# Performance work log

Hardware: AMD Instinct MI355X
Metric: run time of the kernel (lower is better)

The kernel has to match this reference:

```python
import jax, jax.numpy as jnp
import numpy as np


def setup_inputs() -> dict:
    key = jax.random.key(0)
    ks = jax.random.split(key, 8)
    T, S, W, O = 50000, 168, 336, 48
    N = T - W - O + 1
    x = jax.random.uniform(ks[0], (T,), minval=0.5, maxval=1.5, dtype=jnp.float32)
    noise = jax.random.normal(ks[1], (N, W), dtype=jnp.float32) * 0.001  # Normal(0, std=0.001)
    level_sc = jax.random.uniform(ks[2], (), minval=-1.0, maxval=1.0, dtype=jnp.float32)
    seas_sc = jax.random.uniform(ks[3], (), minval=-1.0, maxval=1.0, dtype=jnp.float32)
    init_seas = jax.random.uniform(ks[4], (S,), minval=0.65, maxval=1.35, dtype=jnp.float32)
    W1 = jax.random.normal(ks[5], (W, W), dtype=jnp.float32) / np.float32(np.sqrt(W))
    b1 = jnp.zeros((W,), jnp.float32)
    W2 = jax.random.normal(ks[6], (W, O), dtype=jnp.float32) / np.float32(np.sqrt(W))
    b2 = jnp.zeros((O,), jnp.float32)
    return {"x": x, "noise": noise, "level_sc": level_sc, "seas_sc": seas_sc,
            "init_seas": init_seas, "W1": W1, "b1": b1, "W2": W2, "b2": b2,
            "window_size": W, "out_size": O, "lvp": 1}


def reference(x, noise, level_sc, seas_sc, init_seas, W1, b1, W2, b2,
              window_size, out_size, lvp):
    T = x.shape[0]
    a = jax.nn.sigmoid(level_sc)      # level smoothing coeff
    g = jax.nn.sigmoid(seas_sc)       # seasonal smoothing coeff
    s0 = jnp.exp(init_seas)           # [S] initial multiplicative seasonals
    # seasonals list in torch: seas[0..S-1]=s0, seas[S]=s0[0], seas[S+i]=w_i.
    # Ring buffer holds seas[i..i+S-1] at step i (starting i=1): [s0[1:], s0[0]].
    buf0 = jnp.concatenate([s0[1:], s0[:1]])
    level0 = x[0] / s0[0]

    def step(carry, xi):
        level, buf = carry
        seas_i = buf[0]
        new_level = a * xi / seas_i + (1.0 - a) * level
        new_w = g * xi / new_level + (1.0 - g) * seas_i
        new_buf = jnp.concatenate([buf[1:], new_w[None]])
        return (new_level, new_buf), (new_level, new_w, jnp.log(new_level / level))

    _, (lvls, ws, logdiffs) = jax.lax.scan(step, (level0, buf0), x[1:])
    levels = jnp.concatenate([level0[None], lvls])        # [T]
    seas_full = jnp.concatenate([s0, s0[:1], ws])         # [S+T]

    d = logdiffs[1:] - logdiffs[:-1]
    level_var_loss = jnp.mean(d * d) * lvp

    N = T - window_size - out_size + 1
    idx_in = jnp.arange(N)[:, None] + jnp.arange(window_size)[None, :]   # [N,W]
    idx_lab = jnp.arange(N)[:, None] + window_size + jnp.arange(out_size)[None, :]  # [N,O]
    lev = levels[jnp.arange(N) + window_size][:, None]    # [N,1]
    inp = jnp.log(x[idx_in] / (lev * seas_full[idx_in])) + noise   # noisy squashed inputs
    labels = jnp.log(x[idx_lab] / (lev * seas_full[idx_lab]))

    h = jnp.tanh(inp @ W1 + b1)        # tanh_no_lstm: Linear(336,336)+tanh
    out = h @ W2 + b2                  # linear_no_lstm: Linear(336,48)
    return out, labels, level_var_loss
```

## Files before the change

### kernel.cpp

```cpp
#include <hip/hip_runtime.h>
#include <hip/hip_bf16.h>

typedef __attribute__((ext_vector_type(8))) short  s16x8;
typedef __attribute__((ext_vector_type(4))) short  s16x4;
typedef __attribute__((ext_vector_type(4))) float  f32x4;

#define T_LEN 50000
#define S_LEN 168
#define W_IN  336
#define O_OUT 48
#define N_ROWS (T_LEN - W_IN - O_OUT + 1)
#define N_PAD  49664
#define NBLK   (N_PAD / 64)

__device__ inline short f2bf(float f) {
    union { float f; unsigned u; } v; v.f = f;
    unsigned u = v.u;
    unsigned r = u + 0x7fffu + ((u >> 16) & 1u);
    return (short)(r >> 16);
}

__device__ inline int bfpk(float lo, float hi) {
    float2 f2; f2.x = lo; f2.y = hi;
    __hip_bfloat162 h = __float22bfloat162_rn(f2);
    int r; __builtin_memcpy(&r, &h, 4);
    return r;
}

__device__ inline float readlane_f(float v, int l) {
    return __int_as_float(__builtin_amdgcn_readlane(__float_as_int(v), l));
}

__device__ inline float fast_tanh(float v) {
    float e = __expf(2.f * v);
    return 1.f - 2.f * __builtin_amdgcn_rcpf(e + 1.f);
}

__global__ void k_preconvert(const float* __restrict__ W1, const float* __restrict__ W2,
                             short* __restrict__ W1T, short* __restrict__ W2T,
                             float* __restrict__ S1) {
    int idx = blockIdx.x * 256 + threadIdx.x;
    const int n1 = 352 * 352;
    const int n2 = n1 + 48 * 360;
    if (idx < n1) {
        int j = idx / 352, k = idx % 352;
        W1T[idx] = (j < 336 && k < 336) ? f2bf(W1[k * 336 + j]) : (short)0;
    } else if (idx < n2) {
        int i2 = idx - n1;
        int o = i2 / 360, k = i2 % 360;
        W2T[i2] = (k < 336) ? f2bf(W2[k * 48 + o]) : (short)0;
    } else if (idx < n2 + 352) {
        int j = idx - n2;
        float s = 0.f;
        if (j < 336)
            for (int k = 0; k < 336; ++k) s += W1[k * 336 + j];
        S1[j] = s;
    }
}

#define DPP_FMA(q_, CTRL, W, RM) { \
    int t_ = __builtin_amdgcn_update_dpp(0, __float_as_int(q_), (CTRL), (RM), 0xf, true); \
    q_ = fmaf((W), __int_as_float(t_), q_); }

__global__ void k_scan(const float* __restrict__ x, const float* __restrict__ level_sc,
                       const float* __restrict__ seas_sc, const float* __restrict__ init_seas,
                       float* __restrict__ lw, float* __restrict__ seasinit) {
    int lane = threadIdx.x;
    float a = 1.f / (1.f + expf(-level_sc[0]));
    float g = 1.f / (1.f + expf(-seas_sc[0]));
    float om = 1.f - a, omg = 1.f - g;

    for (int t = lane; t <= S_LEN; t += 64)
        seasinit[t] = expf(init_seas[t < S_LEN ? t : 0]);

    float lpv = x[0] / expf(init_seas[0]);
    if (lane == 0) { lw[0] = lpv; lw[1] = 1.f; }

    float om1 = om, om2v = om1 * om1, om4 = om2v * om2v, om8 = om4 * om4;
    float pl    = powf(om, (float)(lane + 1));
    float fpre  = powf(om, (float)((lane & 15) + 1));
    float fpre2 = powf(om, (float)((lane & 31) + 1));

    int  idx4 = ((lane + 24) & 63) << 2;
    bool lowj = (lane < 40);

#define SCAN(QOUT, XV, RSV) { \
    float q_ = a * (XV) * (RSV); \
    DPP_FMA(q_, 0x111, om1,  0xf); \
    DPP_FMA(q_, 0x112, om2v, 0xf); \
    DPP_FMA(q_, 0x114, om4,  0xf); \
    DPP_FMA(q_, 0x118, om8,  0xf); \
    DPP_FMA(q_, 0x142, fpre,  0xa); \
    DPP_FMA(q_, 0x143, fpre2, 0xc); \
    QOUT = q_; }

#define XLOAD(I) float xr##I = x[1 + 64 * I + lane];
    XLOAD(0) XLOAD(1) XLOAD(2) XLOAD(3) XLOAD(4) XLOAD(5) XLOAD(6) XLOAD(7)
    XLOAD(8) XLOAD(9) XLOAD(10) XLOAD(11) XLOAD(12) XLOAD(13) XLOAD(14) XLOAD(15)
#undef XLOAD

    float sW = expf(init_seas[1 + lane]);
    float sN = expf(init_seas[65 + lane]);
    int t105 = 105 + lane;
    float wPrev = expf(init_seas[t105 >= S_LEN ? 0 : t105]);
    float Qcur; SCAN(Qcur, xr0, __builtin_amdgcn_rcpf(sW));
    int ib = 1;

#define BODY(R, RN, CLAMP) { \
    float lvl = fmaf(pl, lpv, Qcur); \
    lpv = readlane_f(lvl, 63); \
    float w_ = fmaf(omg, sW, (g * xr##R) * __builtin_amdgcn_rcpf(lvl)); \
    float2 pk_; pk_.x = lvl; pk_.y = w_; \
    *(float2*)&lw[2 * (ib + lane)] = pk_; \
    int tA_ = __builtin_amdgcn_ds_bpermute(idx4, __float_as_int(wPrev)); \
    int tB_ = __builtin_amdgcn_ds_bpermute(idx4, __float_as_int(w_)); \
    float sNN_ = lowj ? __int_as_float(tA_) : __int_as_float(tB_); \
    float Qn_; SCAN(Qn_, xr##RN, __builtin_amdgcn_rcpf(sN)); \
    int pidx = ib + 1024 + lane; \
    if (CLAMP) pidx = pidx > (T_LEN - 1) ? (T_LEN - 1) : pidx; \
    xr##R = x[pidx]; \
    Qcur = Qn_; sW = sN; sN = sNN_; wPrev = w_; \
    ib += 64; }

    for (int kb = 0; kb < 47; ++kb) {
        BODY(0,1,0)  BODY(1,2,0)  BODY(2,3,0)  BODY(3,4,0)
        BODY(4,5,0)  BODY(5,6,0)  BODY(6,7,0)  BODY(7,8,0)
        BODY(8,9,0)  BODY(9,10,0) BODY(10,11,0) BODY(11,12,0)
        BODY(12,13,0) BODY(13,14,0) BODY(14,15,0) BODY(15,0,0)
    }
    BODY(0,1,0)  BODY(1,2,0)  BODY(2,3,0)  BODY(3,4,0)
    BODY(4,5,0)  BODY(5,6,0)  BODY(6,7,0)  BODY(7,8,0)
    BODY(8,9,0)  BODY(9,10,0) BODY(10,11,0) BODY(11,12,0)
    BODY(12,13,0)
    BODY(13,14,1) BODY(14,15,1) BODY(15,0,1)
    BODY(0,1,1)  BODY(1,2,1)  BODY(2,3,1)  BODY(3,4,1)
    BODY(4,5,1)  BODY(5,6,1)  BODY(6,7,1)  BODY(7,8,1)
    BODY(8,9,1)  BODY(9,10,1) BODY(10,11,1) BODY(11,12,1)
#undef BODY

    {
        float lvl = fmaf(pl, lpv, Qcur);
        lpv = readlane_f(lvl, 63);
        float w_ = fmaf(omg, sW, (g * xr12) * __builtin_amdgcn_rcpf(lvl));
        float2 pk_; pk_.x = lvl; pk_.y = w_;
        *(float2*)&lw[2 * (49921 + lane)] = pk_;
    }
    {
        float Qn_; SCAN(Qn_, xr13, __builtin_amdgcn_rcpf(sN));
        float lvl = fmaf(pl, lpv, Qn_);
        if (lane < 15) {
            float w_ = fmaf(omg, sN, (g * xr13) * __builtin_amdgcn_rcpf(lvl));
            float2 pk_; pk_.x = lvl; pk_.y = w_;
            *(float2*)&lw[2 * (49985 + lane)] = pk_;
        }
    }
#undef SCAN
}

__global__ void k_logs(const float* __restrict__ x, const float* __restrict__ lw,
                       const float* __restrict__ seasinit,
                       float* __restrict__ F, float* __restrict__ llev,
                       float* __restrict__ partials) {
    __shared__ float sm[258];
    __shared__ float red[256];
    int tid = threadIdx.x;
    int t = blockIdx.x * 256 + tid;
    float ll = 0.f;
    if (t < T_LEN) {
        float2 cur = *(const float2*)&lw[2 * t];
        int ps = t - S_LEN; if (ps < 0) ps = 0;
        float sv = (t <= S_LEN) ? seasinit[t] : lw[2 * ps + 1];
        F[t]  = __logf(x[t]) - __logf(sv);
        ll    = __logf(cur.x);
        llev[t] = ll;
    }
    sm[tid] = ll;
    if (tid < 2) {
        int te = blockIdx.x * 256 + 256 + tid;
        sm[256 + tid] = (te < T_LEN) ? __logf(lw[2 * te]) : 0.f;
    }
    __syncthreads();
    float s = 0.f;
    if (t < T_LEN - 2) {
        float d = sm[tid + 2] - 2.f * sm[tid + 1] + sm[tid];
        s = d * d;
    }
    red[tid] = s; __syncthreads();
    for (int off = 128; off > 0; off >>= 1) {
        if (tid < off) red[tid] += red[tid + off];
        __syncthreads();
    }
    if (tid == 0) partials[blockIdx.x] = red[0];
}

__global__ __launch_bounds__(512, 4) void k_gemm(
        const float* __restrict__ noise, const float* __restrict__ F,
        const float* __restrict__ llev, const short* __restrict__ W1T,
        const float* __restrict__ b1, const short* __restrict__ W2T,
        const float* __restrict__ b2, const float* __restrict__ S1,
        const float* __restrict__ partials, const int* __restrict__ lvp,
        float* __restrict__ out, float* __restrict__ labels, float* __restrict__ loss) {
    __shared__ __align__(16) short hlds[64][360];
    __shared__ __align__(16) float Flds[448];
    __shared__ __align__(16) float Llds[64];
    __shared__ __align__(16) float b1lds[352];
    __shared__ __align__(16) float S1lds[352];

    int t = threadIdx.x, w = t >> 6, l = t & 63;
    int lm = l & 15, lq = l >> 4;
    long n0 = (long)blockIdx.x * 64;

    if (blockIdx.x == 0 && w == 7) {
        float s = partials[l] + partials[l + 64] + partials[l + 128];
        if (l < 4) s += partials[l + 192];
#pragma unroll
        for (int off = 32; off > 0; off >>= 1) s += __shfl_down(s, off, 64);
        if (l == 0) loss[0] = s / (float)(T_LEN - 2) * (float)lvp[0];
    }

    if (t < 112)      *(f32x4*)&Flds[t * 4] = *(const f32x4*)&F[n0 + t * 4];
    else if (t < 128) *(f32x4*)&Llds[(t - 112) * 4] = *(const f32x4*)&llev[n0 + W_IN + (t - 112) * 4];
    else if (t < 216) {
        int i4 = (t - 128) * 4;
        f32x4 v = (f32x4){0.f, 0.f, 0.f, 0.f};
        if (i4 < W_IN) v = *(const f32x4*)&b1[i4];
        *(f32x4*)&b1lds[i4] = v;
    } else if (t < 304) {
        int i4 = (t - 216) * 4;
        *(f32x4*)&S1lds[i4] = *(const f32x4*)&S1[i4];
    }

    int rbase = (w >> 1) * 16;
    int jbase = (w & 1) * 176;
    long an0 = n0 + rbase + lm; if (an0 > N_ROWS - 2) an0 = N_ROWS - 2;
    const float* nr0 = noise + an0 * W_IN + lq * 8;

    f32x4 nc0 = *(const f32x4*)&nr0[0], nc1 = *(const f32x4*)&nr0[4];

    f32x4 acc[11];
#pragma unroll
    for (int c = 0; c < 11; ++c) acc[c] = (f32x4){0.f, 0.f, 0.f, 0.f};

    const short* w1row = &W1T[(jbase + lm) * 352 + lq * 8];
#define LDW(CT, KS) (*(const s16x8*)&w1row[(CT) * 5632 + (KS) * 32])
    s16x8 af0 = LDW(0,0), af1 = LDW(1,0), af2 = LDW(2,0), af3 = LDW(3,0), af4 = LDW(4,0),
          af5 = LDW(5,0), af6 = LDW(6,0), af7 = LDW(7,0), af8 = LDW(8,0), af9 = LDW(9,0),
          af10 = LDW(10,0);

    __syncthreads();

#define MM(CT, AF) acc[CT] = __builtin_amdgcn_mfma_f32_16x16x32_bf16(AF, bf0, acc[CT], 0, 0, 0);

#define KSTEP(KS) { \
    s16x8 bf0; \
    { int fb = rbase + lm + (KS) * 32 + lq * 8; \
      int* b0i = (int*)&bf0; \
      b0i[0] = bfpk(Flds[fb+0] + nc0[0], Flds[fb+1] + nc0[1]); \
      b0i[1] = bfpk(Flds[fb+2] + nc0[2], Flds[fb+3] + nc0[3]); \
      b0i[2] = bfpk(Flds[fb+4] + nc1[0], Flds[fb+5] + nc1[1]); \
      b0i[3] = bfpk(Flds[fb+6] + nc1[2], Flds[fb+7] + nc1[3]); } \
    if ((KS) < 10) { \
      nc0 = *(const f32x4*)&nr0[((KS)+1)*32]; \
      nc1 = *(const f32x4*)&nr0[((KS)+1)*32+4]; \
    } \
    MM(0, af0)   if ((KS) < 10) af0  = LDW(0,  (KS)+1); \
    MM(1, af1)   if ((KS) < 10) af1  = LDW(1,  (KS)+1); \
    MM(2, af2)   if ((KS) < 10) af2  = LDW(2,  (KS)+1); \
    MM(3, af3)   if ((KS) < 10) af3  = LDW(3,  (KS)+1); \
    MM(4, af4)   if ((KS) < 10) af4  = LDW(4,  (KS)+1); \
    MM(5, af5)   if ((KS) < 10) af5  = LDW(5,  (KS)+1); \
    MM(6, af6)   if ((KS) < 10) af6  = LDW(6,  (KS)+1); \
    MM(7, af7)   if ((KS) < 10) af7  = LDW(7,  (KS)+1); \
    MM(8, af8)   if ((KS) < 10) af8  = LDW(8,  (KS)+1); \
    MM(9, af9)   if ((KS) < 10) af9  = LDW(9,  (KS)+1); \
    MM(10, af10) if ((KS) < 10) af10 = LDW(10, (KS)+1); \
}

    KSTEP(0) KSTEP(1) KSTEP(2) KSTEP(3) KSTEP(4) KSTEP(5)
    KSTEP(6) KSTEP(7) KSTEP(8) KSTEP(9) KSTEP(10)
#undef KSTEP
#undef MM
#undef LDW

    float lv0 = Llds[rbase + lm];
#pragma unroll
    for (int ct = 0; ct < 11; ++ct) {
        f32x4 b1q = *(f32x4*)&b1lds[jbase + ct * 16 + lq * 4];
        f32x4 s1q = *(f32x4*)&S1lds[jbase + ct * 16 + lq * 4];
        int2 p0;
        p0.x = bfpk(fast_tanh(fmaf(-lv0, s1q[0], acc[ct][0] + b1q[0])),
                    fast_tanh(fmaf(-lv0, s1q[1], acc[ct][1] + b1q[1])));
        p0.y = bfpk(fast_tanh(fmaf(-lv0, s1q[2], acc[ct][2] + b1q[2])),
                    fast_tanh(fmaf(-lv0, s1q[3], acc[ct][3] + b1q[3])));
        *(int2*)&hlds[rbase + lm][jbase + ct * 16 + lq * 4] = p0;
    }
    __syncthreads();

    if (w < 4) {
        f32x4 a2[3];
        a2[0] = (f32x4){0,0,0,0}; a2[1] = (f32x4){0,0,0,0}; a2[2] = (f32x4){0,0,0,0};
#pragma unroll
        for (int ks = 0; ks < 11; ++ks) {
            s16x8 hf = *(s16x8*)&hlds[w * 16 + lm][ks * 32 + lq * 8];
#pragma unroll
            for (int ct = 0; ct < 3; ++ct) {
                s16x8 bf2 = *(const s16x8*)&W2T[(ct * 16 + lm) * 360 + ks * 32 + lq * 8];
                a2[ct] = __builtin_amdgcn_mfma_f32_16x16x32_bf16(hf, bf2, a2[ct], 0, 0, 0);
            }
        }
        int rloc = w * 16 + lq * 4;
#pragma unroll
        for (int ct = 0; ct < 3; ++ct) {
            float b2v = b2[ct * 16 + lm];
#pragma unroll
            for (int r = 0; r < 4; ++r) {
                long row = n0 + rloc + r;
                if (row < N_ROWS) out[row * O_OUT + ct * 16 + lm] = a2[ct][r] + b2v;
            }
        }
    } else {
        int rb2 = (w - 4) * 16;
        int lrow = l >> 2, cbase = (l & 3) * 12;
        long row = n0 + rb2 + lrow;
        if (row < N_ROWS) {
            float fl = -Llds[rb2 + lrow];
            const float* fp = &Flds[rb2 + lrow + W_IN + cbase];
            float* lp = &labels[row * O_OUT + cbase];
#pragma unroll
            for (int i = 0; i < 12; ++i) lp[i] = fp[i] + fl;
        }
    }
}

extern "C" void kernel_launch(void* const* d_in, const int* in_sizes, int n_in,
                              void* d_out, int out_size, void* d_ws, size_t ws_size,
                              hipStream_t stream) {
    const float* x         = (const float*)d_in[0];
    const float* noise     = (const float*)d_in[1];
    const float* level_sc  = (const float*)d_in[2];
    const float* seas_sc   = (const float*)d_in[3];
    const float* init_seas = (const float*)d_in[4];
    const float* W1        = (const float*)d_in[5];
    const float* b1        = (const float*)d_in[6];
    const float* W2        = (const float*)d_in[7];
    const float* b2        = (const float*)d_in[8];
    const int*   lvp       = (const int*)d_in[11];

    float* out    = (float*)d_out;
    float* labels = out + (long)N_ROWS * O_OUT;
    float* loss   = labels + (long)N_ROWS * O_OUT;

    float* wsf      = (float*)d_ws;
    float* lw       = wsf;
    float* seasinit = wsf + 100096;
    float* F        = wsf + 100288;
    float* llev     = wsf + 150464;
    float* partials = wsf + 200512;
    float* S1f      = wsf + 200768;
    short* W1T      = (short*)(wsf + 201152);
    short* W2T      = W1T + 352 * 352;

    k_preconvert<<<554, 256, 0, stream>>>(W1, W2, W1T, W2T, S1f);
    k_scan<<<1, 64, 0, stream>>>(x, level_sc, seas_sc, init_seas, lw, seasinit);
    k_logs<<<196, 256, 0, stream>>>(x, lw, seasinit, F, llev, partials);
    k_gemm<<<NBLK, 512, 0, stream>>>(noise, F, llev, W1T, b1, W2T, b2, S1f,
                                     partials, lvp, out, labels, loss);
}
```

Before: 162.0 us.

## Split input prep into separate bf16 materialization kernel and register-block GEMM over two row tiles

Adds a k_prep kernel that builds the noisy log inputs (level subtracted) as a padded bf16 matrix in workspace and writes labels. k_gemm then loads bf16 A fragments directly, uses 256 threads with each wave computing two 16-row tiles so every W1 fragment is reused across two MFMAs, and rotates six weight registers instead of eleven. The S1 column-sum correction is dropped because the level term is now folded into the input. This costs an extra global write and read of about 35 MB of bf16 input plus one more launch, in exchange for less conversion work inside the GEMM and less weight reload per row.

```diff
diff --git a/kernel.cpp b/kernel.cpp
--- a/kernel.cpp
+++ b/kernel.cpp
@@ -37,8 +37,7 @@
 }
 
 __global__ void k_preconvert(const float* __restrict__ W1, const float* __restrict__ W2,
-                             short* __restrict__ W1T, short* __restrict__ W2T,
-                             float* __restrict__ S1) {
+                             short* __restrict__ W1T, short* __restrict__ W2T) {
     int idx = blockIdx.x * 256 + threadIdx.x;
     const int n1 = 352 * 352;
     const int n2 = n1 + 48 * 360;
@@ -49,12 +48,6 @@
         int i2 = idx - n1;
         int o = i2 / 360, k = i2 % 360;
         W2T[i2] = (k < 336) ? f2bf(W2[k * 48 + o]) : (short)0;
-    } else if (idx < n2 + 352) {
-        int j = idx - n2;
-        float s = 0.f;
-        if (j < 336)
-            for (int k = 0; k < 336; ++k) s += W1[k * 336 + j];
-        S1[j] = s;
     }
 }
 
@@ -193,24 +186,66 @@
     if (tid == 0) partials[blockIdx.x] = red[0];
 }
 
-__global__ __launch_bounds__(512, 4) void k_gemm(
+__global__ __launch_bounds__(256) void k_prep(
         const float* __restrict__ noise, const float* __restrict__ F,
-        const float* __restrict__ llev, const short* __restrict__ W1T,
+        const float* __restrict__ llev, short* __restrict__ inpbf,
+        float* __restrict__ labels) {
+    __shared__ float Flds[448];
+    __shared__ float Llds[64];
+    int t = threadIdx.x;
+    long n0 = (long)blockIdx.x * 64;
+    if (t < 112)      *(f32x4*)&Flds[t * 4] = *(const f32x4*)&F[n0 + t * 4];
+    else if (t < 128) *(f32x4*)&Llds[(t - 112) * 4] = *(const f32x4*)&llev[n0 + W_IN + (t - 112) * 4];
+    __syncthreads();
+
+    int r = t >> 2, q = t & 3;
+    long n = n0 + r;
+    bool valid = (n < N_ROWS);
+    float lv = Llds[r];
+    const float* nrow = noise + n * (long)W_IN;
+    short* orow = inpbf + n * 352;
+
+#pragma unroll
+    for (int i = 0; i < 11; ++i) {
+        int k0 = q * 88 + i * 8;
+        int4 s = {0, 0, 0, 0};
+        if (valid && k0 < W_IN) {
+            f32x4 nz0 = *(const f32x4*)&nrow[k0];
+            f32x4 nz1 = *(const f32x4*)&nrow[k0 + 4];
+            const float* fp = &Flds[r + k0];
+            s.x = bfpk(fp[0] - lv + nz0[0], fp[1] - lv + nz0[1]);
+            s.y = bfpk(fp[2] - lv + nz0[2], fp[3] - lv + nz0[3]);
+            s.z = bfpk(fp[4] - lv + nz1[0], fp[5] - lv + nz1[1]);
+            s.w = bfpk(fp[6] - lv + nz1[2], fp[7] - lv + nz1[3]);
+        }
+        *(int4*)&orow[k0] = s;
+    }
+    if (valid) {
+#pragma unroll
+        for (int i = 0; i < 3; ++i) {
+            int c = q * 12 + i * 4;
+            const float* fp = &Flds[r + W_IN + c];
+            f32x4 v;
+            v[0] = fp[0] - lv; v[1] = fp[1] - lv; v[2] = fp[2] - lv; v[3] = fp[3] - lv;
+            *(f32x4*)&labels[n * O_OUT + c] = v;
+        }
+    }
+}
+
+__global__ __launch_bounds__(256, 3) void k_gemm(
+        const short* __restrict__ inpbf, const short* __restrict__ W1T,
         const float* __restrict__ b1, const short* __restrict__ W2T,
-        const float* __restrict__ b2, const float* __restrict__ S1,
-        const float* __restrict__ partials, const int* __restrict__ lvp,
-        float* __restrict__ out, float* __restrict__ labels, float* __restrict__ loss) {
+        const float* __restrict__ b2, const float* __restrict__ partials,
+        const int* __restrict__ lvp, float* __restrict__ out,
+        float* __restrict__ loss) {
     __shared__ __align__(16) short hlds[64][360];
-    __shared__ __align__(16) float Flds[448];
-    __shared__ __align__(16) float Llds[64];
     __shared__ __align__(16) float b1lds[352];
-    __shared__ __align__(16) float S1lds[352];
 
     int t = threadIdx.x, w = t >> 6, l = t & 63;
     int lm = l & 15, lq = l >> 4;
     long n0 = (long)blockIdx.x * 64;
 
-    if (blockIdx.x == 0 && w == 7) {
+    if (blockIdx.x == 0 && w == 3) {
         float s = partials[l] + partials[l + 64] + partials[l + 128];
         if (l < 4) s += partials[l + 192];
 #pragma unroll
@@ -218,116 +253,101 @@
         if (l == 0) loss[0] = s / (float)(T_LEN - 2) * (float)lvp[0];
     }
 
-    if (t < 112)      *(f32x4*)&Flds[t * 4] = *(const f32x4*)&F[n0 + t * 4];
-    else if (t < 128) *(f32x4*)&Llds[(t - 112) * 4] = *(const f32x4*)&llev[n0 + W_IN + (t - 112) * 4];
-    else if (t < 216) {
-        int i4 = (t - 128) * 4;
+    if (t < 88) {
+        int i4 = t * 4;
         f32x4 v = (f32x4){0.f, 0.f, 0.f, 0.f};
         if (i4 < W_IN) v = *(const f32x4*)&b1[i4];
         *(f32x4*)&b1lds[i4] = v;
-    } else if (t < 304) {
-        int i4 = (t - 216) * 4;
-        *(f32x4*)&S1lds[i4] = *(const f32x4*)&S1[i4];
-    }
-
-    int rbase = (w >> 1) * 16;
+    }
+
+    int rbase = (w >> 1) * 32;
     int jbase = (w & 1) * 176;
-    long an0 = n0 + rbase + lm; if (an0 > N_ROWS - 2) an0 = N_ROWS - 2;
-    const float* nr0 = noise + an0 * W_IN + lq * 8;
-
-    f32x4 nc0 = *(const f32x4*)&nr0[0], nc1 = *(const f32x4*)&nr0[4];
-
-    f32x4 acc[11];
-#pragma unroll
-    for (int c = 0; c < 11; ++c) acc[c] = (f32x4){0.f, 0.f, 0.f, 0.f};
+    const short* arow0 = inpbf + (n0 + rbase + lm) * 352 + lq * 8;
+    const short* arow1 = arow0 + 16 * 352;
+
+    f32x4 acc0[11], acc1[11];
+#pragma unroll
+    for (int c = 0; c < 11; ++c) { acc0[c] = (f32x4){0,0,0,0}; acc1[c] = (f32x4){0,0,0,0}; }
 
     const short* w1row = &W1T[(jbase + lm) * 352 + lq * 8];
 #define LDW(CT, KS) (*(const s16x8*)&w1row[(CT) * 5632 + (KS) * 32])
-    s16x8 af0 = LDW(0,0), af1 = LDW(1,0), af2 = LDW(2,0), af3 = LDW(3,0), af4 = LDW(4,0),
-          af5 = LDW(5,0), af6 = LDW(6,0), af7 = LDW(7,0), af8 = LDW(8,0), af9 = LDW(9,0),
-          af10 = LDW(10,0);
+    s16x8 af0 = LDW(0,0), af1 = LDW(1,0), af2 = LDW(2,0),
+          af3 = LDW(3,0), af4 = LDW(4,0), af5 = LDW(5,0);
+    s16x8 bA0 = *(const s16x8*)&arow0[0];
+    s16x8 bA1 = *(const s16x8*)&arow1[0];
+
+#define MM2(CT, AF) \
+    acc0[CT] = __builtin_amdgcn_mfma_f32_16x16x32_bf16(AF, b0, acc0[CT], 0, 0, 0); \
+    acc1[CT] = __builtin_amdgcn_mfma_f32_16x16x32_bf16(AF, bb1, acc1[CT], 0, 0, 0);
+
+#define KSTEP_R(KS, A0,A1,A2,A3,A4,A5) { \
+    s16x8 b0 = bA0, bb1 = bA1; \
+    if ((KS) < 10) { \
+        bA0 = *(const s16x8*)&arow0[((KS)+1) * 32]; \
+        bA1 = *(const s16x8*)&arow1[((KS)+1) * 32]; \
+    } \
+    MM2(0, A0)   A0 = LDW(6, (KS)); \
+    MM2(1, A1)   A1 = LDW(7, (KS)); \
+    MM2(2, A2)   A2 = LDW(8, (KS)); \
+    MM2(3, A3)   A3 = LDW(9, (KS)); \
+    MM2(4, A4)   A4 = LDW(10, (KS)); \
+    MM2(5, A5)   if ((KS) < 10) A5 = LDW(0, (KS)+1); \
+    MM2(6, A0)   if ((KS) < 10) A0 = LDW(1, (KS)+1); \
+    MM2(7, A1)   if ((KS) < 10) A1 = LDW(2, (KS)+1); \
+    MM2(8, A2)   if ((KS) < 10) A2 = LDW(3, (KS)+1); \
+    MM2(9, A3)   if ((KS) < 10) A3 = LDW(4, (KS)+1); \
+    MM2(10, A4)  if ((KS) < 10) A4 = LDW(5, (KS)+1); \
+}
+
+    KSTEP_R(0,  af0,af1,af2,af3,af4,af5)
+    KSTEP_R(1,  af5,af0,af1,af2,af3,af4)
+    KSTEP_R(2,  af4,af5,af0,af1,af2,af3)
+    KSTEP_R(3,  af3,af4,af5,af0,af1,af2)
+    KSTEP_R(4,  af2,af3,af4,af5,af0,af1)
+    KSTEP_R(5,  af1,af2,af3,af4,af5,af0)
+    KSTEP_R(6,  af0,af1,af2,af3,af4,af5)
+    KSTEP_R(7,  af5,af0,af1,af2,af3,af4)
+    KSTEP_R(8,  af4,af5,af0,af1,af2,af3)
+    KSTEP_R(9,  af3,af4,af5,af0,af1,af2)
+    KSTEP_R(10, af2,af3,af4,af5,af0,af1)
+#undef KSTEP_R
+#undef MM2
+#undef LDW
 
     __syncthreads();
 
-#define MM(CT, AF) acc[CT] = __builtin_amdgcn_mfma_f32_16x16x32_bf16(AF, bf0, acc[CT], 0, 0, 0);
-
-#define KSTEP(KS) { \
-    s16x8 bf0; \
-    { int fb = rbase + lm + (KS) * 32 + lq * 8; \
-      int* b0i = (int*)&bf0; \
-      b0i[0] = bfpk(Flds[fb+0] + nc0[0], Flds[fb+1] + nc0[1]); \
-      b0i[1] = bfpk(Flds[fb+2] + nc0[2], Flds[fb+3] + nc0[3]); \
-      b0i[2] = bfpk(Flds[fb+4] + nc1[0], Flds[fb+5] + nc1[1]); \
-      b0i[3] = bfpk(Flds[fb+6] + nc1[2], Flds[fb+7] + nc1[3]); } \
-    if ((KS) < 10) { \
-      nc0 = *(const f32x4*)&nr0[((KS)+1)*32]; \
-      nc1 = *(const f32x4*)&nr0[((KS)+1)*32+4]; \
-    } \
-    MM(0, af0)   if ((KS) < 10) af0  = LDW(0,  (KS)+1); \
-    MM(1, af1)   if ((KS) < 10) af1  = LDW(1,  (KS)+1); \
-    MM(2, af2)   if ((KS) < 10) af2  = LDW(2,  (KS)+1); \
-    MM(3, af3)   if ((KS) < 10) af3  = LDW(3,  (KS)+1); \
-    MM(4, af4)   if ((KS) < 10) af4  = LDW(4,  (KS)+1); \
-    MM(5, af5)   if ((KS) < 10) af5  = LDW(5,  (KS)+1); \
-    MM(6, af6)   if ((KS) < 10) af6  = LDW(6,  (KS)+1); \
-    MM(7, af7)   if ((KS) < 10) af7  = LDW(7,  (KS)+1); \
-    MM(8, af8)   if ((KS) < 10) af8  = LDW(8,  (KS)+1); \
-    MM(9, af9)   if ((KS) < 10) af9  = LDW(9,  (KS)+1); \
-    MM(10, af10) if ((KS) < 10) af10 = LDW(10, (KS)+1); \
-}
-
-    KSTEP(0) KSTEP(1) KSTEP(2) KSTEP(3) KSTEP(4) KSTEP(5)
-    KSTEP(6) KSTEP(7) KSTEP(8) KSTEP(9) KSTEP(10)
-#undef KSTEP
-#undef MM
-#undef LDW
-
-    float lv0 = Llds[rbase + lm];
 #pragma unroll
     for (int ct = 0; ct < 11; ++ct) {
         f32x4 b1q = *(f32x4*)&b1lds[jbase + ct * 16 + lq * 4];
-        f32x4 s1q = *(f32x4*)&S1lds[jbase + ct * 16 + lq * 4];
-        int2 p0;
-        p0.x = bfpk(fast_tanh(fmaf(-lv0, s1q[0], acc[ct][0] + b1q[0])),
-                    fast_tanh(fmaf(-lv0, s1q[1], acc[ct][1] + b1q[1])));
-        p0.y = bfpk(fast_tanh(fmaf(-lv0, s1q[2], acc[ct][2] + b1q[2])),
-                    fast_tanh(fmaf(-lv0, s1q[3], acc[ct][3] + b1q[3])));
-        *(int2*)&hlds[rbase + lm][jbase + ct * 16 + lq * 4] = p0;
+        int2 p0, p1;
+        p0.x = bfpk(fast_tanh(acc0[ct][0] + b1q[0]), fast_tanh(acc0[ct][1] + b1q[1]));
+        p0.y = bfpk(fast_tanh(acc0[ct][2] + b1q[2]), fast_tanh(acc0[ct][3] + b1q[3]));
+        p1.x = bfpk(fast_tanh(acc1[ct][0] + b1q[0]), fast_tanh(acc1[ct][1] + b1q[1]));
+        p1.y = bfpk(fast_tanh(acc1[ct][2] + b1q[2]), fast_tanh(acc1[ct][3] + b1q[3]));
+        *(int2*)&hlds[rbase + lm][jbase + ct * 16 + lq * 4]      = p0;
+        *(int2*)&hlds[rbase + 16 + lm][jbase + ct * 16 + lq * 4] = p1;
     }
     __syncthreads();
 
-    if (w < 4) {
-        f32x4 a2[3];
-        a2[0] = (f32x4){0,0,0,0}; a2[1] = (f32x4){0,0,0,0}; a2[2] = (f32x4){0,0,0,0};
-#pragma unroll
-        for (int ks = 0; ks < 11; ++ks) {
-            s16x8 hf = *(s16x8*)&hlds[w * 16 + lm][ks * 32 + lq * 8];
-#pragma unroll
-            for (int ct = 0; ct < 3; ++ct) {
-                s16x8 bf2 = *(const s16x8*)&W2T[(ct * 16 + lm) * 360 + ks * 32 + lq * 8];
-                a2[ct] = __builtin_amdgcn_mfma_f32_16x16x32_bf16(hf, bf2, a2[ct], 0, 0, 0);
-            }
-        }
-        int rloc = w * 16 + lq * 4;
+    f32x4 a2[3];
+    a2[0] = (f32x4){0,0,0,0}; a2[1] = (f32x4){0,0,0,0}; a2[2] = (f32x4){0,0,0,0};
+#pragma unroll
+    for (int ks = 0; ks < 11; ++ks) {
+        s16x8 hf = *(s16x8*)&hlds[w * 16 + lm][ks * 32 + lq * 8];
 #pragma unroll
         for (int ct = 0; ct < 3; ++ct) {
-            float b2v = b2[ct * 16 + lm];
-#pragma unroll
-            for (int r = 0; r < 4; ++r) {
-                long row = n0 + rloc + r;
-                if (row < N_ROWS) out[row * O_OUT + ct * 16 + lm] = a2[ct][r] + b2v;
-            }
-        }
-    } else {
-        int rb2 = (w - 4) * 16;
-        int lrow = l >> 2, cbase = (l & 3) * 12;
-        long row = n0 + rb2 + lrow;
-        if (row < N_ROWS) {
-            float fl = -Llds[rb2 + lrow];
-            const float* fp = &Flds[rb2 + lrow + W_IN + cbase];
-            float* lp = &labels[row * O_OUT + cbase];
-#pragma unroll
-            for (int i = 0; i < 12; ++i) lp[i] = fp[i] + fl;
+            s16x8 bf2 = *(const s16x8*)&W2T[(ct * 16 + lm) * 360 + ks * 32 + lq * 8];
+            a2[ct] = __builtin_amdgcn_mfma_f32_16x16x32_bf16(hf, bf2, a2[ct], 0, 0, 0);
+        }
+    }
+    int rloc = w * 16 + lq * 4;
+#pragma unroll
+    for (int ct = 0; ct < 3; ++ct) {
+        float b2v = b2[ct * 16 + lm];
+#pragma unroll
+        for (int r = 0; r < 4; ++r) {
+            long row = n0 + rloc + r;
+            if (row < N_ROWS) out[row * O_OUT + ct * 16 + lm] = a2[ct][r] + b2v;
         }
     }
 }
@@ -356,13 +376,13 @@
     float* F        = wsf + 100288;
     float* llev     = wsf + 150464;
     float* partials = wsf + 200512;
-    float* S1f      = wsf + 200768;
-    short* W1T      = (short*)(wsf + 201152);
+    short* W1T      = (short*)(wsf + 200768);
     short* W2T      = W1T + 352 * 352;
-
-    k_preconvert<<<554, 256, 0, stream>>>(W1, W2, W1T, W2T, S1f);
+    short* inpbf    = (short*)(wsf + 271360);
+
+    k_preconvert<<<552, 256, 0, stream>>>(W1, W2, W1T, W2T);
     k_scan<<<1, 64, 0, stream>>>(x, level_sc, seas_sc, init_seas, lw, seasinit);
     k_logs<<<196, 256, 0, stream>>>(x, lw, seasinit, F, llev, partials);
-    k_gemm<<<NBLK, 512, 0, stream>>>(noise, F, llev, W1T, b1, W2T, b2, S1f,
-                                     partials, lvp, out, labels, loss);
-}
+    k_prep<<<NBLK, 256, 0, stream>>>(noise, F, llev, inpbf, labels);
+    k_gemm<<<NBLK, 256, 0, stream>>>(inpbf, W1T, b1, W2T, b2, partials, lvp, out, loss);
+}
```

New measurement: 193.3 us. 1.19x slower.
